# Kernel tuning notes

Measured on AMD Instinct MI355X. Metric: run time of the kernel, lower is better.

The kernel has to match this reference:

```python
import math
import jax, jax.numpy as jnp
import numpy as np

B, S, D, H = 8, 512, 1024, 16
DH = D // H
NEG_BIG = -1.0e30  # stands in for torch's -np.inf (exp underflows to 0 identically)


def setup_inputs() -> dict:
    key0 = jax.random.key(0)
    ks = jax.random.split(key0, 20)
    n = lambda k, shp, s=1.0: jax.random.normal(k, shp, dtype=jnp.float32) * s
    inp = {}
    inp["query"] = n(ks[0], (B, S, D))
    inp["key"] = n(ks[1], (B, S, D))
    inp["value"] = n(ks[2], (B, S, D))
    # rel has exact zeros (they get masked to -10000 before its softmax)
    inp["rel"] = jax.random.randint(ks[3], (B, S, S), 0, 3).astype(jnp.float32)
    inp["timestamp"] = n(ks[4], (B, S, S))
    inp["l1"] = jnp.float32(0.3)
    inp["l2"] = jnp.float32(0.3)
    # causal mask: True = masked (future positions)
    inp["mask"] = jnp.broadcast_to(jnp.triu(jnp.ones((S, S), dtype=bool), k=1), (B, S, S))
    inp["encode_pos"] = 0
    # three qkv projection linears (total_size -> total_size)
    w = 1.0 / math.sqrt(D)
    inp["Wq"], inp["bq"] = n(ks[5], (D, D), w), jnp.zeros((D,), jnp.float32)
    inp["Wk"], inp["bk"] = n(ks[6], (D, D), w), jnp.zeros((D,), jnp.float32)
    inp["Wv"], inp["bv"] = n(ks[7], (D, D), w), jnp.zeros((D,), jnp.float32)
    # clip_factor / guessing_factor: Linear(head_size -> 1) applied to per-head key
    wh = 1.0 / math.sqrt(DH)
    inp["Wc"], inp["bc"] = n(ks[8], (1, DH), wh), jnp.zeros((1,), jnp.float32)
    inp["Wg"], inp["bg"] = n(ks[9], (1, DH), wh), jnp.zeros((1,), jnp.float32)
    return inp


def reference(query, key, value, rel, timestamp, l1, l2, mask, encode_pos,
              Wq, bq, Wk, bk, Wv, bv, Wc, bc, Wg, bg):
    b, s, d = query.shape
    dh = Wc.shape[1]
    h = d // dh

    def proj(x, W, bias):  # [b,s,d] -> [b,h,s,dh]
        return (x @ W.T + bias).reshape(b, s, h, dh).transpose(0, 2, 1, 3)

    q = proj(query, Wq, bq)
    k = proj(key, Wk, bk)
    v = proj(value, Wv, bv)

    m4 = mask[:, None]          # [b,1,s,s] broadcast over heads
    rel4 = rel[:, None]         # [b,1,s,s]
    ts4 = timestamp[:, None]    # [b,1,s,s]

    # relative softmax: zeros masked to -10000
    rel_attn = jax.nn.softmax(jnp.where(rel4 == 0, -10000.0, rel4), axis=-1)

    # scaled dot-product scores
    scores = jnp.einsum('bhqd,bhkd->bhqk', q, k) / math.sqrt(dh)
    scores = jnp.where(m4, -1.0e9, scores)

    # clip / guessing factors from per-head key -> [b,h,s,1]
    cf = k @ Wc.T + bc
    gf = k @ Wg.T + bg
    R1 = jax.nn.sigmoid(gf - cf) + gf

    # time-decay softmax
    time_stamp = jnp.where(m4, NEG_BIG, jnp.exp(-jnp.abs(ts4)))
    Rs = time_stamp + R1  # [b,h,s,s] (R1 broadcasts over last axis, as in torch)

    prob_attn = jax.nn.softmax(scores, axis=-1)
    time_attn = jax.nn.softmax(Rs, axis=-1)
    prob_attn = (1.0 - l2) * prob_attn + l2 * time_attn
    prob_attn = (1.0 - l1) * prob_attn + l1 * rel_attn

    out = jnp.einsum('bhqk,bhkd->bhqd', prob_attn, v)
    out = out.transpose(0, 2, 1, 3).reshape(b, s, d)
    return out, prob_attn
```

## Files before the change

kernel.cpp:

```cpp
#include <hip/hip_runtime.h>
#include <math.h>

typedef __attribute__((ext_vector_type(8))) short short8;
typedef __attribute__((ext_vector_type(4))) float f32x4;

#define B_  8
#define S_  512
#define D_  1024
#define H_  16
#define DH_ 64

__device__ __forceinline__ unsigned short f2bf(float f) {
    unsigned int u = __float_as_uint(f);
    u += 0x7FFFu + ((u >> 16) & 1u);
    return (unsigned short)(u >> 16);
}
__device__ __forceinline__ float bf2f(unsigned short u) {
    return __uint_as_float(((unsigned int)u) << 16);
}
__device__ __forceinline__ unsigned cvtpk(float lo, float hi) {
    unsigned r;
    asm("v_cvt_pk_bf16_f32 %0, %1, %2" : "=v"(r) : "v"(lo), "v"(hi));
    return r;
}
__device__ __forceinline__ void gload_lds16(const void* g, void* l) {
    __builtin_amdgcn_global_load_lds(
        (const __attribute__((address_space(1))) unsigned int*)g,
        (__attribute__((address_space(3))) unsigned int*)l, 16, 0, 0);
}

__global__ __launch_bounds__(256) void conv_w(
    const float* __restrict__ wq, const float* __restrict__ wk, const float* __restrict__ wv,
    unsigned short* __restrict__ Wbf)
{
    const size_t NW = 262144;
    for (size_t i4 = (size_t)blockIdx.x*blockDim.x + threadIdx.x; i4 < 3*NW;
         i4 += (size_t)gridDim.x*blockDim.x) {
        const int z = (int)(i4 / NW);
        const float* s = (z == 0) ? wq : (z == 1) ? wk : wv;
        const size_t off = i4 - (size_t)z*NW;
        const float4 f = ((const float4*)s)[off];
        ushort4 u; u.x = f2bf(f.x); u.y = f2bf(f.y); u.z = f2bf(f.z); u.w = f2bf(f.w);
        ((ushort4*)(Wbf + (size_t)z*NW*4))[off] = u;
    }
}

__global__ __launch_bounds__(256) void qkv_gemm(
    const float* __restrict__ Aq, const float* __restrict__ Ak, const float* __restrict__ Av,
    const unsigned short* __restrict__ Wbf,
    const float* __restrict__ bq, const float* __restrict__ bk, const float* __restrict__ bv,
    unsigned short* __restrict__ qw, unsigned short* __restrict__ kw,
    unsigned short* __restrict__ vtw)
{
    __shared__ float As[128][64];
    __shared__ unsigned short Bs[128][64];

    const int bid = blockIdx.x;
    const int wid = (bid & 7) * 96 + (bid >> 3);
    const int z   = wid >> 8;
    const int rem = wid & 255;
    const int bm  = (rem >> 3) * 128;
    const int bn  = (rem & 7) * 128;

    const float* A = (z == 0) ? Aq : (z == 1) ? Ak : Av;
    const unsigned short* W = Wbf + (size_t)z * 1048576;
    const float* bias = (z == 0) ? bq : (z == 1) ? bk : bv;
    const float scale = (z == 0) ? 0.125f : 1.0f;

    const int t = threadIdx.x, w = t >> 6, l = t & 63, lr = l & 15, lg = l >> 4;
    const int wr = (w >> 1) * 64, wc = (w & 1) * 64;

    const int srowA = t >> 4, sblkA = t & 15;
    const float* AstA = A + (size_t)(bm + srowA) * 1024 + 4 * (sblkA ^ (srowA & 7));
    const int srowW = t >> 3;
    const int scolW = 8 * ((t & 7) ^ (srowW & 7));
    const unsigned short* Wst = W + (size_t)(bn + srowW) * 1024 + scolW;
    char* AsB = (char*)As; char* BsB = (char*)Bs;
    const float4* Af = (const float4*)As;

    f32x4 acc[4][4] = {};
    for (int k0 = 0; k0 < 1024; k0 += 64) {
        __syncthreads();
        #pragma unroll
        for (int j = 0; j < 8; j++)
            gload_lds16(AstA + (size_t)(16*j)*1024 + k0, AsB + 4096*j + t*16);
        #pragma unroll
        for (int j = 0; j < 4; j++)
            gload_lds16(Wst + (size_t)(32*j)*1024 + k0, BsB + 4096*j + t*16);
        __syncthreads();
        #pragma unroll
        for (int s = 0; s < 2; s++) {
            short8 af[4], bf4[4];
            #pragma unroll
            for (int i = 0; i < 4; i++) {
                const int row = wr + 16*i + lr;
                const int b0 = 8*s + 2*lg;
                const float4 lo = Af[row*16 + (b0      ^ (row & 7))];
                const float4 hi = Af[row*16 + ((b0+1)  ^ (row & 7))];
                union { uint4 u; short8 s8; } cv;
                cv.u.x = cvtpk(lo.x, lo.y); cv.u.y = cvtpk(lo.z, lo.w);
                cv.u.z = cvtpk(hi.x, hi.y); cv.u.w = cvtpk(hi.z, hi.w);
                af[i] = cv.s8;
            }
            #pragma unroll
            for (int j = 0; j < 4; j++) {
                const int row = wc + 16*j + lr;
                bf4[j] = *(const short8*)(BsB + row*128 + (((4*s + lg) ^ (row & 7)) << 4));
            }
            #pragma unroll
            for (int i = 0; i < 4; i++)
                #pragma unroll
                for (int j = 0; j < 4; j++)
                    acc[i][j] = __builtin_amdgcn_mfma_f32_16x16x32_bf16(af[i], bf4[j], acc[i][j], 0, 0, 0);
        }
    }

    if (z < 2) {
        unsigned short* outp = (z == 0) ? qw : kw;
        #pragma unroll
        for (int j = 0; j < 4; j++) {
            const int n = bn + wc + 16*j + lr;
            const float bvx = bias[n];
            const int h = n >> 6, dh = n & 63;
            #pragma unroll
            for (int i = 0; i < 4; i++)
                #pragma unroll
                for (int r = 0; r < 4; r++) {
                    const int m = bm + wr + 16*i + 4*lg + r;
                    const int bb = m >> 9, s = m & 511;
                    outp[(((size_t)(bb*H_ + h))*S_ + s)*DH_ + dh] = f2bf((acc[i][j][r] + bvx) * scale);
                }
        }
    } else {
        #pragma unroll
        for (int j = 0; j < 4; j++) {
            const int n = bn + wc + 16*j + lr;
            const float bvx = bias[n];
            const int h = n >> 6, dh = n & 63;
            #pragma unroll
            for (int i = 0; i < 4; i++) {
                const int m0 = bm + wr + 16*i + 4*lg;
                const int bb = m0 >> 9, s0 = m0 & 511;
                ushort4 u;
                u.x = f2bf(acc[i][j][0] + bvx); u.y = f2bf(acc[i][j][1] + bvx);
                u.z = f2bf(acc[i][j][2] + bvx); u.w = f2bf(acc[i][j][3] + bvx);
                *(ushort4*)&vtw[(((size_t)(bb*H_ + h))*DH_ + dh)*S_ + s0] = u;
            }
        }
    }
}

__global__ __launch_bounds__(256) void e_kernel(
    const float* __restrict__ rel, const float* __restrict__ tsp,
    const float* __restrict__ pl1, const float* __restrict__ pl2,
    unsigned short* __restrict__ E)
{
    const int t = threadIdx.x, w = t >> 6, l = t & 63;
    const int ridx = blockIdx.x * 4 + w;
    const int q = ridx & (S_ - 1);
    const float l1 = *pl1, l2 = *pl2;
    const float c_t = (1.f - l1) * l2, c_r = l1;
    const float* tr = tsp + (size_t)ridx * S_;
    const float* rr = rel + (size_t)ridx * S_;

    float tv[8], rv[8]; float st = 0.f, sr = 0.f;
    #pragma unroll
    for (int j = 0; j < 8; j++) {
        const int k = l + 64*j;
        const float rvv = rr[k];
        rv[j] = (rvv != 0.f) ? __expf(rvv) : 0.f;
        sr += rv[j];
        float tvv = 0.f;
        if (k <= q) tvv = __expf(__expf(-fabsf(tr[k])));
        tv[j] = tvv; st += tvv;
    }
    #pragma unroll
    for (int m = 32; m; m >>= 1) { st += __shfl_xor(st, m); sr += __shfl_xor(sr, m); }
    const float ti   = c_t / st;
    const float riv  = (sr > 0.f) ? c_r / sr : 0.f;
    const float runi = (sr > 0.f) ? 0.f : c_r / (float)S_;

    unsigned short* Er = E + (size_t)ridx * S_;
    #pragma unroll
    for (int j = 0; j < 8; j++) {
        const int k = l + 64*j;
        Er[k] = f2bf(tv[j]*ti + rv[j]*riv + runi);
    }
}

__global__ __launch_bounds__(256) void attn_mfma(
    const unsigned short* __restrict__ qw, const unsigned short* __restrict__ kw,
    const unsigned short* __restrict__ vtw, const unsigned short* __restrict__ E,
    const float* __restrict__ pl1, const float* __restrict__ pl2,
    float* __restrict__ out, float* __restrict__ prob)
{
    __shared__ unsigned short Ps[2][64][72];

    const int t = threadIdx.x, w = t >> 6, l = t & 63, lr = l & 15, lg = l >> 4;
    const int bid = blockIdx.x;
    const int j   = bid >> 3;
    const int bh  = (bid & 7) * 16 + (j & 15);
    const int b   = bh >> 4, h = bh & 15;
    const int q0  = (j >> 4) * 64;
    const float l1 = *pl1, l2 = *pl2;
    const float c_p = (1.f - l1) * (1.f - l2);
    const unsigned short* qp = qw + (size_t)bh * (S_ * DH_);
    const unsigned short* kp = kw + (size_t)bh * (S_ * DH_);
    const unsigned short* vt = vtw + (size_t)bh * (DH_ * S_);

    short8 qa[2];
    #pragma unroll
    for (int s = 0; s < 2; s++)
        qa[s] = *(const short8*)&qp[(size_t)(q0 + 16*w + lr)*DH_ + 32*s + 8*lg];

    const int qrb = q0 + 16*w + 4*lg;

    unsigned int scp[8][4][2];
    #pragma unroll
    for (int ch = 0; ch < 8; ch++) {
        f32x4 a4[4] = {};
        #pragma unroll
        for (int s = 0; s < 2; s++)
            #pragma unroll
            for (int g = 0; g < 4; g++) {
                const short8 kb = *(const short8*)&kp[(size_t)(ch*64 + 16*g + lr)*DH_ + 32*s + 8*lg];
                a4[g] = __builtin_amdgcn_mfma_f32_16x16x32_bf16(qa[s], kb, a4[g], 0, 0, 0);
            }
        #pragma unroll
        for (int g = 0; g < 4; g++) {
            const int k = 64*ch + 16*g + lr;
            const float v0 = (k <= qrb + 0) ? a4[g][0] : -1e30f;
            const float v1 = (k <= qrb + 1) ? a4[g][1] : -1e30f;
            const float v2 = (k <= qrb + 2) ? a4[g][2] : -1e30f;
            const float v3 = (k <= qrb + 3) ? a4[g][3] : -1e30f;
            scp[ch][g][0] = ((unsigned)f2bf(v1) << 16) | f2bf(v0);
            scp[ch][g][1] = ((unsigned)f2bf(v3) << 16) | f2bf(v2);
        }
    }

    float mx[4] = {-1e30f, -1e30f, -1e30f, -1e30f};
    #pragma unroll
    for (int ch = 0; ch < 8; ch++)
        #pragma unroll
        for (int g = 0; g < 4; g++) {
            const unsigned u0 = scp[ch][g][0], u1 = scp[ch][g][1];
            mx[0] = fmaxf(mx[0], __uint_as_float(u0 << 16));
            mx[1] = fmaxf(mx[1], __uint_as_float(u0 & 0xffff0000u));
            mx[2] = fmaxf(mx[2], __uint_as_float(u1 << 16));
            mx[3] = fmaxf(mx[3], __uint_as_float(u1 & 0xffff0000u));
        }
    #pragma unroll
    for (int i = 0; i < 4; i++)
        #pragma unroll
        for (int m = 8; m; m >>= 1) mx[i] = fmaxf(mx[i], __shfl_xor(mx[i], m));

    float sm[4] = {0.f, 0.f, 0.f, 0.f};
    #pragma unroll
    for (int ch = 0; ch < 8; ch++)
        #pragma unroll
        for (int g = 0; g < 4; g++) {
            const unsigned u0 = scp[ch][g][0], u1 = scp[ch][g][1];
            const float e0 = __expf(__uint_as_float(u0 << 16)          - mx[0]);
            const float e1 = __expf(__uint_as_float(u0 & 0xffff0000u) - mx[1]);
            const float e2 = __expf(__uint_as_float(u1 << 16)          - mx[2]);
            const float e3 = __expf(__uint_as_float(u1 & 0xffff0000u) - mx[3]);
            sm[0] += e0; sm[1] += e1; sm[2] += e2; sm[3] += e3;
            scp[ch][g][0] = ((unsigned)f2bf(e1) << 16) | f2bf(e0);
            scp[ch][g][1] = ((unsigned)f2bf(e3) << 16) | f2bf(e2);
        }
    #pragma unroll
    for (int i = 0; i < 4; i++)
        #pragma unroll
        for (int m = 8; m; m >>= 1) sm[i] += __shfl_xor(sm[i], m);
    float pinv[4];
    #pragma unroll
    for (int i = 0; i < 4; i++) pinv[i] = c_p / sm[i];

    f32x4 pv[4] = {};
    const unsigned short* Eb = E + ((size_t)b * S_ + qrb) * S_;
    const int prow = 16*w + 4*lg;
    const int rr = 16*w + ((l >> 2) & 15), cg = (l & 3) << 4;

    #pragma unroll
    for (int ch = 0; ch < 8; ch++) {
        const int p = ch & 1;
        #pragma unroll
        for (int g = 0; g < 4; g++) {
            const int kc = 16*g + lr;
            const unsigned u0 = scp[ch][g][0], u1 = scp[ch][g][1];
            const size_t eb = (size_t)(64*ch + kc);
            Ps[p][prow + 0][kc] = f2bf(__uint_as_float(u0 << 16)          * pinv[0] + bf2f(Eb[eb]));
            Ps[p][prow + 1][kc] = f2bf(__uint_as_float(u0 & 0xffff0000u) * pinv[1] + bf2f(Eb[eb + 512]));
            Ps[p][prow + 2][kc] = f2bf(__uint_as_float(u1 << 16)          * pinv[2] + bf2f(Eb[eb + 1024]));
            Ps[p][prow + 3][kc] = f2bf(__uint_as_float(u1 & 0xffff0000u) * pinv[3] + bf2f(Eb[eb + 1536]));
        }
        #pragma unroll
        for (int s = 0; s < 2; s++) {
            const short8 pa = *(const short8*)&Ps[p][16*w + lr][32*s + 8*lg];
            #pragma unroll
            for (int g = 0; g < 4; g++) {
                const short8 vb = *(const short8*)&vt[(size_t)(16*g + lr)*S_ + 64*ch + 32*s + 8*lg];
                pv[g] = __builtin_amdgcn_mfma_f32_16x16x32_bf16(pa, vb, pv[g], 0, 0, 0);
            }
        }
        {
            const unsigned short* psr = &Ps[p][rr][cg];
            float* prp = prob + ((size_t)bh * S_ + q0 + rr) * S_ + 64*ch + cg;
            #pragma unroll
            for (int jj = 0; jj < 4; jj++) {
                f32x4 f;
                f.x = bf2f(psr[4*jj + 0]); f.y = bf2f(psr[4*jj + 1]);
                f.z = bf2f(psr[4*jj + 2]); f.w = bf2f(psr[4*jj + 3]);
                *(f32x4*)&prp[4*jj] = f;
            }
        }
    }

    #pragma unroll
    for (int g = 0; g < 4; g++)
        #pragma unroll
        for (int i = 0; i < 4; i++)
            out[((size_t)(b*S_ + qrb + i))*D_ + h*DH_ + 16*g + lr] = pv[g][i];
}

extern "C" void kernel_launch(void* const* d_in, const int* in_sizes, int n_in,
                              void* d_out, int out_size, void* d_ws, size_t ws_size,
                              hipStream_t stream)
{
    const float* query = (const float*)d_in[0];
    const float* key   = (const float*)d_in[1];
    const float* value = (const float*)d_in[2];
    const float* rel   = (const float*)d_in[3];
    const float* tsp   = (const float*)d_in[4];
    const float* l1    = (const float*)d_in[5];
    const float* l2    = (const float*)d_in[6];
    const float* Wq = (const float*)d_in[9];
    const float* bq = (const float*)d_in[10];
    const float* Wk = (const float*)d_in[11];
    const float* bk = (const float*)d_in[12];
    const float* Wv = (const float*)d_in[13];
    const float* bv = (const float*)d_in[14];

    float* out  = (float*)d_out;
    float* prob = (float*)d_out + (size_t)B_ * S_ * D_;

    const size_t headN = (size_t)B_ * H_ * S_ * DH_;
    unsigned short* Wbf = (unsigned short*)d_ws;
    unsigned short* qw  = Wbf + 3*1048576;
    unsigned short* kw  = qw + headN;
    unsigned short* vtw = kw + headN;
    unsigned short* Ew  = vtw + headN;

    conv_w<<<512, 256, 0, stream>>>(Wq, Wk, Wv, Wbf);

    qkv_gemm<<<768, 256, 0, stream>>>(query, key, value, Wbf,
                                      bq, bk, bv, qw, kw, vtw);

    e_kernel<<<(B_ * S_) / 4, 256, 0, stream>>>(rel, tsp, l1, l2, Ew);

    attn_mfma<<<1024, 256, 0, stream>>>(qw, kw, vtw, Ew, l1, l2, out, prob);
}
```

Measured before the change: 154.7 us.

## Prefetch next E chunk into registers and store probabilities directly from fp32

The next chunk of the bf16 E tile is loaded into registers one iteration early, so global load latency overlaps the current chunk's work. The prob output is now written straight from the fp32 values as they are computed, replacing the pass that read the bf16 shared-memory tile back and widened it before storing. This removes LDS reads and conversions and gives prob full fp32 precision, but the global stores are now scalar, strided 4-byte writes instead of 16-byte vector stores, and the prefetch raises register pressure.

```diff
diff --git a/kernel.cpp b/kernel.cpp
--- a/kernel.cpp
+++ b/kernel.cpp
@@ -278,21 +278,44 @@
 
     f32x4 pv[4] = {};
     const unsigned short* Eb = E + ((size_t)b * S_ + qrb) * S_;
+    float* pr = prob + ((size_t)bh * S_ + qrb) * S_;
     const int prow = 16*w + 4*lg;
-    const int rr = 16*w + ((l >> 2) & 15), cg = (l & 3) << 4;
+
+    unsigned short ecur[4][4];
+    #pragma unroll
+    for (int g = 0; g < 4; g++)
+        #pragma unroll
+        for (int i = 0; i < 4; i++)
+            ecur[g][i] = Eb[(size_t)512*i + 16*g + lr];
 
     #pragma unroll
     for (int ch = 0; ch < 8; ch++) {
         const int p = ch & 1;
+        unsigned short enext[4][4];
+        if (ch < 7) {
+            #pragma unroll
+            for (int g = 0; g < 4; g++)
+                #pragma unroll
+                for (int i = 0; i < 4; i++)
+                    enext[g][i] = Eb[(size_t)512*i + 64*(ch+1) + 16*g + lr];
+        }
         #pragma unroll
         for (int g = 0; g < 4; g++) {
             const int kc = 16*g + lr;
             const unsigned u0 = scp[ch][g][0], u1 = scp[ch][g][1];
             const size_t eb = (size_t)(64*ch + kc);
-            Ps[p][prow + 0][kc] = f2bf(__uint_as_float(u0 << 16)          * pinv[0] + bf2f(Eb[eb]));
-            Ps[p][prow + 1][kc] = f2bf(__uint_as_float(u0 & 0xffff0000u) * pinv[1] + bf2f(Eb[eb + 512]));
-            Ps[p][prow + 2][kc] = f2bf(__uint_as_float(u1 << 16)          * pinv[2] + bf2f(Eb[eb + 1024]));
-            Ps[p][prow + 3][kc] = f2bf(__uint_as_float(u1 & 0xffff0000u) * pinv[3] + bf2f(Eb[eb + 1536]));
+            const float f0 = __uint_as_float(u0 << 16)          * pinv[0] + bf2f(ecur[g][0]);
+            const float f1 = __uint_as_float(u0 & 0xffff0000u) * pinv[1] + bf2f(ecur[g][1]);
+            const float f2 = __uint_as_float(u1 << 16)          * pinv[2] + bf2f(ecur[g][2]);
+            const float f3 = __uint_as_float(u1 & 0xffff0000u) * pinv[3] + bf2f(ecur[g][3]);
+            Ps[p][prow + 0][kc] = f2bf(f0);
+            Ps[p][prow + 1][kc] = f2bf(f1);
+            Ps[p][prow + 2][kc] = f2bf(f2);
+            Ps[p][prow + 3][kc] = f2bf(f3);
+            pr[eb]        = f0;
+            pr[eb + 512]  = f1;
+            pr[eb + 1024] = f2;
+            pr[eb + 1536] = f3;
         }
         #pragma unroll
         for (int s = 0; s < 2; s++) {
@@ -303,16 +326,12 @@
                 pv[g] = __builtin_amdgcn_mfma_f32_16x16x32_bf16(pa, vb, pv[g], 0, 0, 0);
             }
         }
-        {
-            const unsigned short* psr = &Ps[p][rr][cg];
-            float* prp = prob + ((size_t)bh * S_ + q0 + rr) * S_ + 64*ch + cg;
-            #pragma unroll
-            for (int jj = 0; jj < 4; jj++) {
-                f32x4 f;
-                f.x = bf2f(psr[4*jj + 0]); f.y = bf2f(psr[4*jj + 1]);
-                f.z = bf2f(psr[4*jj + 2]); f.w = bf2f(psr[4*jj + 3]);
-                *(f32x4*)&prp[4*jj] = f;
-            }
+        if (ch < 7) {
+            #pragma unroll
+            for (int g = 0; g < 4; g++)
+                #pragma unroll
+                for (int i = 0; i < 4; i++)
+                    ecur[g][i] = enext[g][i];
         }
     }
 
```

After: 148.6 us. -3.9%, faster.
